# Kernel optimization log

Measured on AMD Instinct MI355X. Metric: run time of the kernel, lower is better.

## Reference

```python
import jax, jax.numpy as jnp
import numpy as np

B, N, C = 16, 3136, 576
HEADS, AG, WIN, PS = 8, 49, 56, 7


def setup_inputs() -> dict:
    key = jax.random.key(0)
    ks = jax.random.split(key, 14)
    std = 0.02
    d = {
        "x": jax.random.normal(ks[0], (B, N, C), jnp.float32),
        "Wq": std * jax.random.normal(ks[1], (C, C), jnp.float32),
        "Wkv": std * jax.random.normal(ks[2], (C, 2 * C), jnp.float32),
        "an_bias": std * jax.random.normal(ks[3], (HEADS, AG, 7, 7), jnp.float32),
        "na_bias": std * jax.random.normal(ks[4], (HEADS, AG, 7, 7), jnp.float32),
        "ah_bias": std * jax.random.normal(ks[5], (1, HEADS, AG, WIN, 1), jnp.float32),
        "aw_bias": std * jax.random.normal(ks[6], (1, HEADS, AG, 1, WIN), jnp.float32),
        "ha_bias": std * jax.random.normal(ks[7], (1, HEADS, WIN, 1, AG), jnp.float32),
        "wa_bias": std * jax.random.normal(ks[8], (1, HEADS, 1, WIN, AG), jnp.float32),
        "dwc_w": std * jax.random.normal(ks[9], (C, 1, 3, 3), jnp.float32),  # depthwise 3x3
        "dwc_gamma": jnp.ones((C,), jnp.float32),
        "dwc_beta": jnp.zeros((C,), jnp.float32),
        "proj_w": std * jax.random.normal(ks[10], (C, C), jnp.float32),
        "proj_b": jnp.zeros((C,), jnp.float32),
        "H": 56,
        "W": 56,
    }
    return d


def _forward(x, Wq, Wkv, an_bias, na_bias, ah_bias, aw_bias, ha_bias, wa_bias,
             dwc_w, dwc_gamma, dwc_beta, proj_w, proj_b, H, W):
    b, n, c = x.shape
    heads, ag = an_bias.shape[0], an_bias.shape[1]
    hd = c // heads
    scale = hd ** -0.5

    q = x @ Wq                     # [b, n, c]
    kv = x @ Wkv                   # [b, n, 2c]
    k, v = kv[..., :c], kv[..., c:]

    # agent tokens: adaptive avg pool q (H,W grid) down to (PS, PS)
    ps = int(round(ag ** 0.5))
    qa = q.reshape(b, ps, H // ps, ps, W // ps, c).mean(axis=(2, 4))  # [b, ps, ps, c]
    a = qa.reshape(b, ag, heads, hd).transpose(0, 2, 1, 3)            # [b, h, ag, hd]

    qh = q.reshape(b, n, heads, hd).transpose(0, 2, 1, 3)  # [b, h, n, hd]
    kh = k.reshape(b, n, heads, hd).transpose(0, 2, 1, 3)
    vh = v.reshape(b, n, heads, hd).transpose(0, 2, 1, 3)

    # stage 1: agent attends to K/V, with interpolated + separable position bias
    pb1 = jax.image.resize(an_bias, (heads, ag, H, W), "linear").reshape(1, heads, ag, n)
    pb2 = (ah_bias + aw_bias).reshape(1, heads, ag, n)
    agent_scores = jnp.einsum("bhad,bhnd->bhan", a * scale, kh) + pb1 + pb2
    agent_attn = jax.nn.softmax(agent_scores, axis=-1)
    agent_v = jnp.einsum("bhan,bhnd->bhad", agent_attn, vh)  # [b, h, ag, hd]

    # stage 2: queries attend to agent tokens
    ab1 = jax.image.resize(na_bias, (heads, ag, H, W), "linear").reshape(1, heads, ag, n)
    ab1 = ab1.transpose(0, 1, 3, 2)                                   # [1, h, n, ag]
    ab2 = (ha_bias + wa_bias).reshape(1, heads, n, ag)
    q_scores = jnp.einsum("bhnd,bhad->bhna", qh * scale, a) + ab1 + ab2
    q_attn = jax.nn.softmax(q_scores, axis=-1)
    out = jnp.einsum("bhna,bhad->bhnd", q_attn, agent_v)
    out = out.transpose(0, 2, 1, 3).reshape(b, n, c)

    # depthwise-conv branch on v (DW_bn_relu, BN in eval mode with unit stats)
    vimg = v.transpose(0, 2, 1).reshape(b, c, H, W)
    y = jax.lax.conv_general_dilated(vimg, dwc_w, (1, 1), "SAME",
                                     feature_group_count=c,
                                     dimension_numbers=("NCHW", "OIHW", "NCHW"))
    y = jax.nn.relu(y * dwc_gamma[None, :, None, None] + dwc_beta[None, :, None, None])
    y = y.reshape(b, c, n).transpose(0, 2, 1)

    out = out + y
    out = out @ proj_w + proj_b   # output projection
    return out


def reference(x, Wq, Wkv, an_bias, na_bias, ah_bias, aw_bias, ha_bias, wa_bias,
              dwc_w, dwc_gamma, dwc_beta, proj_w, proj_b, H, W):
    return _forward(x, Wq, Wkv, an_bias, na_bias, ah_bias, aw_bias, ha_bias, wa_bias,
                    dwc_w, dwc_gamma, dwc_beta, proj_w, proj_b, H, W)
```

## Files before the change

kernel.cpp:

```cpp
#include <hip/hip_runtime.h>
#include <stdint.h>

typedef unsigned short u16;
typedef u16   u16x4 __attribute__((ext_vector_type(4)));
typedef u16   u16x8 __attribute__((ext_vector_type(8)));
typedef float f32x4 __attribute__((ext_vector_type(4)));
typedef __bf16 bf16x8 __attribute__((ext_vector_type(8)));

#define BB    16
#define NN    3136
#define CC    576
#define HEADS 8
#define HD    72
#define AGN   49
#define NTOT  1728
#define NCH   7
#define SCALE 0.1178511301977579f

__device__ __forceinline__ u16 f2bf(float f) {
    unsigned u = __float_as_uint(f);
    return (u16)((u + 0x7fffu + ((u >> 16) & 1u)) >> 16);
}
__device__ __forceinline__ float bf2f(u16 u) {
    return __uint_as_float(((unsigned)u) << 16);
}

__global__ __launch_bounds__(256) void k_cast_x(const float* __restrict__ x, u16* __restrict__ xb) {
    size_t i = (size_t)blockIdx.x * 256 + threadIdx.x;
    f32x4 v = *(const f32x4*)(x + i * 4);
    u16x4 o; o[0] = f2bf(v[0]); o[1] = f2bf(v[1]); o[2] = f2bf(v[2]); o[3] = f2bf(v[3]);
    *(u16x4*)(xb + i * 4) = o;
}

__global__ __launch_bounds__(256) void k_prep_w(const float* __restrict__ Wq, const float* __restrict__ Wkv,
                                                const float* __restrict__ Wp,
                                                u16* __restrict__ wbT, u16* __restrict__ wpT) {
    int idx = blockIdx.x * 256 + threadIdx.x;
    if (idx < NTOT * CC) {
        int nn = idx / CC, kk = idx % CC;
        float v = (nn < CC) ? Wq[kk * CC + nn] : Wkv[kk * (2 * CC) + (nn - CC)];
        wbT[idx] = f2bf(v);
    } else {
        int j = idx - NTOT * CC;
        int nn = j / CC, kk = j % CC;
        wpT[j] = f2bf(Wp[kk * CC + nn]);
    }
}

__device__ __forceinline__ float bilerp7(const float* __restrict__ g, int oy, int ox) {
    float cy = (oy - 3.5f) * 0.125f;
    float cx = (ox - 3.5f) * 0.125f;
    float fy0 = floorf(cy), fx0 = floorf(cx);
    float ty = cy - fy0, tx = cx - fx0;
    int iy0 = (int)fy0, ix0 = (int)fx0;
    int y0 = min(6, max(0, iy0)), y1 = min(6, max(0, iy0 + 1));
    int x0 = min(6, max(0, ix0)), x1 = min(6, max(0, ix0 + 1));
    float g00 = g[y0 * 7 + x0], g01 = g[y0 * 7 + x1];
    float g10 = g[y1 * 7 + x0], g11 = g[y1 * 7 + x1];
    return (1.f - ty) * ((1.f - tx) * g00 + tx * g01) + ty * ((1.f - tx) * g10 + tx * g11);
}

__global__ __launch_bounds__(256) void k_bias1(const float* __restrict__ an, const float* __restrict__ ah,
                                               const float* __restrict__ aw, float* __restrict__ b1) {
    int idx = blockIdx.x * 256 + threadIdx.x;
    int ag = idx % AGN; int r = idx / AGN; int n = r % NN; int h = r / NN;
    int y = n / 56, x = n % 56;
    float v = bilerp7(an + (h * AGN + ag) * 49, y, x);
    b1[idx] = v + ah[(h * AGN + ag) * 56 + y] + aw[(h * AGN + ag) * 56 + x];
}

__global__ __launch_bounds__(256) void k_bias2(const float* __restrict__ na, const float* __restrict__ ha,
                                               const float* __restrict__ wa, float* __restrict__ b2p) {
    int idx = blockIdx.x * 256 + threadIdx.x;
    int ag = idx & 63; int r = idx >> 6; int n = r % NN; int h = r / NN;
    float v;
    if (ag < AGN) {
        int y = n / 56, x = n % 56;
        v = bilerp7(na + (h * AGN + ag) * 49, y, x)
          + ha[(h * 56 + y) * AGN + ag] + wa[(h * 56 + x) * AGN + ag];
    } else v = -1e30f;
    b2p[idx] = v;
}

template<int MODE>
__global__ __launch_bounds__(256) void k_gemm(const u16* __restrict__ A, const u16* __restrict__ Bt,
                                              u16* __restrict__ Qp, u16* __restrict__ Kp, u16* __restrict__ Vp,
                                              float* __restrict__ Cf, const float* __restrict__ bias,
                                              const int M) {
    const int NB = (MODE == 0) ? NTOT : CC;
    __shared__ u16 SMEM[2 * 128 * 64];
    u16* Asm = SMEM;
    u16* Bsm = SMEM + 128 * 64;
    const int t = threadIdx.x, lane = t & 63, wid = t >> 6;
    const int wm = wid & 1, wn = wid >> 1;
    const int nwg = gridDim.x * gridDim.y;
    const int id = blockIdx.y * gridDim.x + blockIdx.x;
    const int qq = nwg >> 3, rr = nwg & 7;
    const int xcd = id & 7, off = id >> 3;
    const int nid = (xcd < rr ? xcd * (qq + 1) : rr * (qq + 1) + (xcd - rr) * qq) + off;
    const int row0 = (nid / gridDim.x) * 128, col0 = (nid % gridDim.x) * 128;
    const int lr = lane & 15, lk = lane >> 4;
    f32x4 acc[4][4];
#pragma unroll
    for (int m = 0; m < 4; m++)
#pragma unroll
        for (int n2 = 0; n2 < 4; n2++) acc[m][n2] = (f32x4)0.f;

    for (int kt = 0; kt < 9; ++kt) {
        const int k0 = kt * 64;
#pragma unroll
        for (int it = 0; it < 4; ++it) {
            int flat = it * 256 + wid * 64 + lane;
            int r = flat >> 3, lc = (flat & 7) ^ (r & 7);
            int arow = (MODE == 0) ? (row0 + r) : min(row0 + r, M - 1);
            const u16* src = A + (size_t)arow * CC + k0 + lc * 8;
            __builtin_amdgcn_global_load_lds((const __attribute__((address_space(1))) void*)src,
                                             (__attribute__((address_space(3))) void*)(&Asm[(it * 256 + wid * 64) * 8]),
                                             16, 0, 0);
        }
#pragma unroll
        for (int it = 0; it < 4; ++it) {
            int flat = it * 256 + wid * 64 + lane;
            int r = flat >> 3, lc = (flat & 7) ^ (r & 7);
            int brow = min(col0 + r, NB - 1);
            const u16* src = Bt + (size_t)brow * CC + k0 + lc * 8;
            __builtin_amdgcn_global_load_lds((const __attribute__((address_space(1))) void*)src,
                                             (__attribute__((address_space(3))) void*)(&Bsm[(it * 256 + wid * 64) * 8]),
                                             16, 0, 0);
        }
        __syncthreads();
#pragma unroll
        for (int kk = 0; kk < 2; ++kk) {
            const int klocal2 = (kk * 32 + lk * 8) * 2;
            bf16x8 av[4], bv[4];
#pragma unroll
            for (int m = 0; m < 4; m++) {
                int row = wm * 64 + m * 16 + lr;
                av[m] = *(const bf16x8*)((const char*)Asm + row * 128 + (klocal2 ^ ((row & 7) << 4)));
            }
#pragma unroll
            for (int n2 = 0; n2 < 4; n2++) {
                int row = wn * 64 + n2 * 16 + lr;
                bv[n2] = *(const bf16x8*)((const char*)Bsm + row * 128 + (klocal2 ^ ((row & 7) << 4)));
            }
#pragma unroll
            for (int m = 0; m < 4; m++)
#pragma unroll
                for (int n2 = 0; n2 < 4; n2++)
                    acc[m][n2] = __builtin_amdgcn_mfma_f32_16x16x32_bf16(av[m], bv[n2], acc[m][n2], 0, 0, 0);
        }
        __syncthreads();
    }

    if (MODE == 0) {
#pragma unroll
        for (int ph = 0; ph < 2; ++ph) {
            if (wm == ph) {
#pragma unroll
                for (int m = 0; m < 4; m++)
#pragma unroll
                    for (int n2 = 0; n2 < 4; n2++) {
                        int col = wn * 64 + n2 * 16 + lr;
#pragma unroll
                        for (int j = 0; j < 4; j++)
                            SMEM[(m * 16 + lk * 4 + j) * 136 + col] = f2bf(acc[m][n2][j]);
                    }
            }
            __syncthreads();
#pragma unroll
            for (int cc2 = 0; cc2 < 4; ++cc2) {
                int cidx = cc2 * 256 + t;
                int rl = cidx >> 4, colc = cidx & 15;
                int cgl = col0 + colc * 8;
                if (cgl < NTOT) {
                    u16x8 v = *(const u16x8*)&SMEM[rl * 136 + colc * 8];
                    int rgl = row0 + ph * 64 + rl;
                    int which = cgl / 576, rem = cgl - which * 576;
                    int hh = rem / 72, dd = rem - hh * 72;
                    u16* dst = which == 0 ? Qp : (which == 1 ? Kp : Vp);
                    int b = rgl / NN, n = rgl - b * NN;
                    *(u16x8*)(dst + ((size_t)(b * 8 + hh) * NN + n) * 72 + dd) = v;
                }
            }
            __syncthreads();
        }
    } else {
        float* Ef = (float*)SMEM;
#pragma unroll
        for (int ph = 0; ph < 4; ++ph) {
            if (wm == (ph >> 1)) {
#pragma unroll
                for (int mm = 0; mm < 2; mm++) {
                    int m = (ph & 1) * 2 + mm;
#pragma unroll
                    for (int n2 = 0; n2 < 4; n2++) {
                        int col = wn * 64 + n2 * 16 + lr;
                        float addv = (MODE == 1) ? bias[min(col0 + col, NB - 1)] : 0.f;
#pragma unroll
                        for (int j = 0; j < 4; j++)
                            Ef[(mm * 16 + lk * 4 + j) * 136 + col] = acc[m][n2][j] + addv;
                    }
                }
            }
            __syncthreads();
#pragma unroll
            for (int cc2 = 0; cc2 < 4; ++cc2) {
                int cidx = cc2 * 256 + t;
                int rl = cidx >> 5, colc = cidx & 31;
                int cgl = col0 + colc * 4;
                int rgl = row0 + ph * 32 + rl;
                if (cgl < NB && rgl < M) {
                    f32x4 v = *(const f32x4*)&Ef[rl * 136 + colc * 4];
                    *(f32x4*)(Cf + (size_t)rgl * 576 + cgl) = v;
                }
            }
            __syncthreads();
        }
    }
}

__global__ __launch_bounds__(256) void k_poolx(const u16* __restrict__ xb, u16* __restrict__ px) {
    const int t = threadIdx.x;
    const int b = blockIdx.x / 7, p1 = blockIdx.x % 7;
    for (int task = t; task < 504; task += 256) {
        int p2 = task / 72, c8 = task - p2 * 72;
        const u16* base = xb + ((size_t)b * NN + (p1 * 8) * 56 + p2 * 8) * CC + c8 * 8;
        float s[8] = {0.f, 0.f, 0.f, 0.f, 0.f, 0.f, 0.f, 0.f};
        for (int y = 0; y < 8; ++y)
#pragma unroll
            for (int x = 0; x < 8; ++x) {
                u16x8 v = *(const u16x8*)(base + (size_t)(y * 56 + x) * CC);
#pragma unroll
                for (int j = 0; j < 8; j++) s[j] += bf2f(v[j]);
            }
        u16x8 o;
#pragma unroll
        for (int j = 0; j < 8; j++) o[j] = f2bf(s[j] * 0.015625f);
        *(u16x8*)(px + (size_t)(b * AGN + p1 * 7 + p2) * CC + c8 * 8) = o;
    }
}

__global__ __launch_bounds__(256) void k_stageA(const u16* __restrict__ Kp, const u16* __restrict__ Vp,
                                                const float* __restrict__ a_f, const float* __restrict__ b1,
                                                float* __restrict__ part) {
    const int t = threadIdx.x, lane = t & 63, w = t >> 6;
    const int c = lane & 15, g = lane >> 4;
    const int bh = blockIdx.y, b = bh >> 3, h = bh & 7;
    const int chunk = blockIdx.x;

    __shared__ u16 A_lds[64][104];
    __shared__ u16 K_lds[64][104];
    __shared__ u16 Vt[80][72];
    __shared__ u16 P_lds[64][72];

    for (int i = t; i < 64 * 104; i += 256) {
        int r = i / 104, cc = i - r * 104;
        if (cc >= 72 || r >= 49) A_lds[r][cc] = 0;
        if (cc >= 72) K_lds[r][cc] = 0;
    }
    for (int i = t; i < 8 * 72; i += 256) Vt[72 + i / 72][i % 72] = 0;
    for (int i = t; i < 49 * 72; i += 256) {
        int r = i / 72, d = i - r * 72;
        A_lds[r][d] = f2bf(a_f[(size_t)(b * 49 + r) * CC + h * 72 + d] * SCALE);
    }
    __syncthreads();

    bf16x8 bfA[3];
#pragma unroll
    for (int ks = 0; ks < 3; ++ks) bfA[ks] = *(const bf16x8*)&A_lds[16 * w + c][8 * g + 32 * ks];

    float m_run = -1e30f, l_run = 0.f;
    f32x4 acc[5];
#pragma unroll
    for (int dt = 0; dt < 5; ++dt) acc[dt] = (f32x4)0.f;

    const u16* kb = Kp + ((size_t)(b * 8 + h) * NN + chunk * 448) * 72;
    const u16* vb = Vp + ((size_t)(b * 8 + h) * NN + chunk * 448) * 72;
    const int arow = min(16 * w + c, 48);

    for (int tile = 0; tile < 7; ++tile) {
        for (int i = t; i < 576; i += 256) {
            int nl = i / 9, ch = i - nl * 9;
            u16x8 kd = *(const u16x8*)(kb + (size_t)tile * 4608 + i * 8);
            *(u16x8*)&K_lds[nl][ch * 8] = kd;
        }
        for (int i = t; i < 576; i += 256) {
            int ch = i >> 6, nl = i & 63;
            u16x8 vd = *(const u16x8*)(vb + (size_t)tile * 4608 + (nl * 9 + ch) * 8);
#pragma unroll
            for (int j = 0; j < 8; j++) Vt[ch * 8 + j][nl] = vd[j];
        }
        __syncthreads();

        f32x4 sT[4];
        const int nbase = chunk * 448 + tile * 64 + 4 * g;
#pragma unroll
        for (int nm = 0; nm < 4; ++nm) {
            f32x4 sv;
#pragma unroll
            for (int j = 0; j < 4; j++)
                sv[j] = b1[(size_t)(h * NN + nbase + 16 * nm + j) * AGN + arow];
#pragma unroll
            for (int ks = 0; ks < 3; ++ks) {
                bf16x8 af = *(const bf16x8*)&K_lds[16 * nm + c][8 * g + 32 * ks];
                sv = __builtin_amdgcn_mfma_f32_16x16x32_bf16(af, bfA[ks], sv, 0, 0, 0);
            }
            sT[nm] = sv;
        }

        float mt = sT[0][0];
#pragma unroll
        for (int nm = 0; nm < 4; ++nm)
#pragma unroll
            for (int j = 0; j < 4; j++) mt = fmaxf(mt, sT[nm][j]);
        mt = fmaxf(mt, __shfl_xor(mt, 16, 64));
        mt = fmaxf(mt, __shfl_xor(mt, 32, 64));
        float mnew = fmaxf(m_run, mt);
        float ps = 0.f;
#pragma unroll
        for (int nm = 0; nm < 4; ++nm) {
            float p0 = __expf(sT[nm][0] - mnew);
            float p1 = __expf(sT[nm][1] - mnew);
            float p2 = __expf(sT[nm][2] - mnew);
            float p3 = __expf(sT[nm][3] - mnew);
            ps += (p0 + p1) + (p2 + p3);
            unsigned pk01 = ((unsigned)f2bf(p1) << 16) | f2bf(p0);
            unsigned pk23 = ((unsigned)f2bf(p3) << 16) | f2bf(p2);
            unsigned* dst = (unsigned*)&P_lds[16 * w + c][16 * nm + 4 * g];
            dst[0] = pk01; dst[1] = pk23;
        }
        ps += __shfl_xor(ps, 16, 64);
        ps += __shfl_xor(ps, 32, 64);
        float rsc = __expf(m_run - mnew);
        l_run = l_run * rsc + ps;
        m_run = mnew;

        float rj[4];
#pragma unroll
        for (int j = 0; j < 4; j++) rj[j] = __shfl(rsc, 4 * g + j, 64);
        bf16x8 pa[2];
#pragma unroll
        for (int ks = 0; ks < 2; ++ks) pa[ks] = *(const bf16x8*)&P_lds[16 * w + c][8 * g + 32 * ks];
#pragma unroll
        for (int dt = 0; dt < 5; ++dt) {
            f32x4 a0 = acc[dt];
#pragma unroll
            for (int j = 0; j < 4; j++) a0[j] *= rj[j];
#pragma unroll
            for (int ks = 0; ks < 2; ++ks) {
                bf16x8 vf = *(const bf16x8*)&Vt[16 * dt + c][8 * g + 32 * ks];
                a0 = __builtin_amdgcn_mfma_f32_16x16x32_bf16(pa[ks], vf, a0, 0, 0, 0);
            }
            acc[dt] = a0;
        }
        __syncthreads();
    }

    const size_t pbase = (size_t)(bh * NCH + chunk) * (49 * 74);
#pragma unroll
    for (int dt = 0; dt < 5; ++dt) {
        int d = 16 * dt + c;
        if (d < 72) {
#pragma unroll
            for (int j = 0; j < 4; j++) {
                int agent = 16 * w + 4 * g + j;
                if (agent < 49) part[pbase + agent * 74 + d] = acc[dt][j];
            }
        }
    }
    if (g == 0) {
        int agent = 16 * w + c;
        if (agent < 49) {
            part[pbase + agent * 74 + 72] = m_run;
            part[pbase + agent * 74 + 73] = l_run;
        }
    }
}

__global__ __launch_bounds__(256) void k_reduceA(const float* __restrict__ part, float* __restrict__ agv) {
    const int bh = blockIdx.x, t = threadIdx.x;
    const float* pb = part + (size_t)bh * NCH * (49 * 74);
    for (int idx = t; idx < 49 * 72; idx += 256) {
        int row = idx / 72, d = idx - row * 72;
        float m = -1e30f;
#pragma unroll
        for (int c = 0; c < NCH; c++) m = fmaxf(m, pb[c * (49 * 74) + row * 74 + 72]);
        float accv = 0.f, l = 0.f;
#pragma unroll
        for (int c = 0; c < NCH; c++) {
            const float* pc = pb + c * (49 * 74) + row * 74;
            float e = __expf(pc[72] - m);
            accv += pc[d] * e;
            l += pc[73] * e;
        }
        agv[(size_t)(bh * 49 + row) * 72 + d] = accv / l;
    }
}

__global__ __launch_bounds__(256) void k_stageB(const u16* __restrict__ Qp, const float* __restrict__ a_f,
                                                const float* __restrict__ agv, const float* __restrict__ b2p,
                                                u16* __restrict__ oat) {
    const int t = threadIdx.x, lane = t & 63, w = t >> 6;
    const int c = lane & 15, g = lane >> 4;
    const int bh = blockIdx.y, b = bh >> 3, h = bh & 7;
    const int n0 = blockIdx.x * 256;

    __shared__ u16 A_lds[64][104];
    __shared__ u16 avT[80][72];
    __shared__ u16 Pt[4][64][76];

    for (int i = t; i < 64 * 104; i += 256) {
        int r = i / 104, cc = i - r * 104;
        if (cc >= 72 || r >= 49) A_lds[r][cc] = 0;
    }
    for (int i = t; i < 80 * 72; i += 256) ((u16*)avT)[i] = 0;
    __syncthreads();
    for (int i = t; i < 49 * 72; i += 256) {
        int r = i / 72, d = i - r * 72;
        A_lds[r][d] = f2bf(a_f[(size_t)(b * 49 + r) * CC + h * 72 + d] * SCALE);
        avT[d][r]   = f2bf(agv[(size_t)(bh * 49 + r) * 72 + d]);
    }
    __syncthreads();

    bf16x8 afr[4][3];
#pragma unroll
    for (int mt = 0; mt < 4; ++mt)
#pragma unroll
        for (int ks = 0; ks < 3; ++ks) afr[mt][ks] = *(const bf16x8*)&A_lds[16 * mt + c][8 * g + 32 * ks];

    const int nw0 = n0 + w * 64;
#pragma unroll
    for (int cg = 0; cg < 4; ++cg) {
        const int n = nw0 + 16 * cg + c;
        const int ne = min(n, NN - 1);
        const u16* qp = Qp + ((size_t)(b * 8 + h) * NN + ne) * 72;
        bf16x8 qf[3];
#pragma unroll
        for (int ks = 0; ks < 3; ++ks) qf[ks] = *(const bf16x8*)(qp + 8 * g + 32 * ks);
        const float* bp = b2p + (size_t)(h * NN + ne) * 64;
        f32x4 sv[4];
#pragma unroll
        for (int mt = 0; mt < 4; ++mt) sv[mt] = *(const f32x4*)(bp + 16 * mt + 4 * g);
#pragma unroll
        for (int ks = 0; ks < 3; ++ks)
#pragma unroll
            for (int mt = 0; mt < 4; ++mt)
                sv[mt] = __builtin_amdgcn_mfma_f32_16x16x32_bf16(afr[mt][ks], qf[ks], sv[mt], 0, 0, 0);
        float mx = sv[0][0];
#pragma unroll
        for (int mt = 0; mt < 4; ++mt)
#pragma unroll
            for (int j = 0; j < 4; j++) mx = fmaxf(mx, sv[mt][j]);
        mx = fmaxf(mx, __shfl_xor(mx, 16, 64));
        mx = fmaxf(mx, __shfl_xor(mx, 32, 64));
        float ps = 0.f;
#pragma unroll
        for (int mt = 0; mt < 4; ++mt) {
#pragma unroll
            for (int j = 0; j < 4; j++) { sv[mt][j] = __expf(sv[mt][j] - mx); ps += sv[mt][j]; }
        }
        ps += __shfl_xor(ps, 16, 64);
        ps += __shfl_xor(ps, 32, 64);
        float inv = 1.f / ps;
#pragma unroll
        for (int mt = 0; mt < 4; ++mt) {
            unsigned pk01 = ((unsigned)f2bf(sv[mt][1] * inv) << 16) | f2bf(sv[mt][0] * inv);
            unsigned pk23 = ((unsigned)f2bf(sv[mt][3] * inv) << 16) | f2bf(sv[mt][2] * inv);
            unsigned* dst = (unsigned*)&Pt[w][16 * cg + c][16 * mt + 4 * g];
            dst[0] = pk01; dst[1] = pk23;
        }
    }
    bf16x8 vfr[5][2];
#pragma unroll
    for (int dt = 0; dt < 5; ++dt)
#pragma unroll
        for (int ks = 0; ks < 2; ++ks) vfr[dt][ks] = *(const bf16x8*)&avT[16 * dt + c][8 * g + 32 * ks];
#pragma unroll
    for (int rt = 0; rt < 4; ++rt) {
        bf16x8 pf[2];
#pragma unroll
        for (int ks = 0; ks < 2; ++ks) pf[ks] = *(const bf16x8*)&Pt[w][16 * rt + c][8 * g + 32 * ks];
#pragma unroll
        for (int dt = 0; dt < 5; ++dt) {
            f32x4 a0 = (f32x4)0.f;
            a0 = __builtin_amdgcn_mfma_f32_16x16x32_bf16(pf[0], vfr[dt][0], a0, 0, 0, 0);
            a0 = __builtin_amdgcn_mfma_f32_16x16x32_bf16(pf[1], vfr[dt][1], a0, 0, 0, 0);
            int dd = 16 * dt + c;
            if (dd < 72) {
#pragma unroll
                for (int j = 0; j < 4; j++) {
                    int nn2 = nw0 + 16 * rt + 4 * g + j;
                    if (nn2 < NN) oat[((size_t)b * NN + nn2) * CC + h * 72 + dd] = f2bf(a0[j]);
                }
            }
        }
    }
}

__global__ __launch_bounds__(576) void k_conv(const u16* __restrict__ Vp, const u16* __restrict__ oat,
                                              const float* __restrict__ w, const float* __restrict__ gamma,
                                              const float* __restrict__ beta, u16* __restrict__ pre) {
    const int t = threadIdx.x;
    const int g8 = t % 72;
    const int p  = t / 72;
    const int c0 = g8 * 8;
    const int hh = c0 / 72, dl = c0 - hh * 72;

    __shared__ float wlds[CC * 9];
    __shared__ float glds[CC], blds[CC];
    for (int i = t; i < CC * 9; i += 576) wlds[i] = w[i];
    glds[t < CC ? t : 0] = gamma[t < CC ? t : 0];
    blds[t < CC ? t : 0] = beta[t < CC ? t : 0];
    __syncthreads();

    float wv[8][9], gm[8], bt[8];
#pragma unroll
    for (int j = 0; j < 8; j++) {
#pragma unroll
        for (int tap = 0; tap < 9; tap++) wv[j][tap] = wlds[(c0 + j) * 9 + tap];
        gm[j] = glds[c0 + j]; bt[j] = blds[c0 + j];
    }

    for (int pt = blockIdx.x * 8 + p; pt < BB * NN; pt += gridDim.x * 8) {
        int b = pt / NN, n = pt - b * NN;
        int y = n / 56, x = n % 56;
        const u16* vbase = Vp + ((size_t)(b * 8 + hh) * NN) * 72 + dl;
        float a[8] = {0.f, 0.f, 0.f, 0.f, 0.f, 0.f, 0.f, 0.f};
#pragma unroll
        for (int dy = -1; dy <= 1; ++dy) {
            int yy = y + dy; if (yy < 0 || yy > 55) continue;
#pragma unroll
            for (int dx = -1; dx <= 1; ++dx) {
                int xx = x + dx; if (xx < 0 || xx > 55) continue;
                u16x8 vv = *(const u16x8*)(vbase + (size_t)(yy * 56 + xx) * 72);
                int tap = (dy + 1) * 3 + (dx + 1);
#pragma unroll
                for (int j = 0; j < 8; j++) a[j] += bf2f(vv[j]) * wv[j][tap];
            }
        }
        u16x8 ov = *(const u16x8*)(oat + (size_t)pt * CC + c0);
        u16x8 rr;
#pragma unroll
        for (int j = 0; j < 8; j++)
            rr[j] = f2bf(bf2f(ov[j]) + fmaxf(a[j] * gm[j] + bt[j], 0.f));
        *(u16x8*)(pre + (size_t)pt * CC + c0) = rr;
    }
}

extern "C" void kernel_launch(void* const* d_in, const int* in_sizes, int n_in,
                              void* d_out, int out_size, void* d_ws, size_t ws_size,
                              hipStream_t stream) {
    const float* x     = (const float*)d_in[0];
    const float* Wq    = (const float*)d_in[1];
    const float* Wkv   = (const float*)d_in[2];
    const float* an_b  = (const float*)d_in[3];
    const float* na_b  = (const float*)d_in[4];
    const float* ah_b  = (const float*)d_in[5];
    const float* aw_b  = (const float*)d_in[6];
    const float* ha_b  = (const float*)d_in[7];
    const float* wa_b  = (const float*)d_in[8];
    const float* dwcw  = (const float*)d_in[9];
    const float* gam   = (const float*)d_in[10];
    const float* bet   = (const float*)d_in[11];
    const float* projw = (const float*)d_in[12];
    const float* projb = (const float*)d_in[13];
    float* out = (float*)d_out;

    char* ws = (char*)d_ws;
    u16* wbT  = (u16*)(ws + 0);
    u16* wpT  = (u16*)(ws + 1990656);
    u16* xb   = (u16*)(ws + 2654208);
    u16* Qp   = (u16*)(ws + 60456960);
    u16* Kp   = (u16*)(ws + 118259712);
    u16* Vp   = (u16*)(ws + 176062464);
    float* af = (float*)(ws + 233865216);
    u16* px   = (u16*)(ws + 235671552);
    float* agv= (float*)(ws + 235671552);
    float* b1 = (float*)(ws + 237477888);
    float* b2p= (float*)(ws + 242395136);
    float* part = (float*)xb;
    u16* obuf = Kp;

    k_cast_x<<<28224, 256, 0, stream>>>(x, xb);
    k_prep_w<<<5184, 256, 0, stream>>>(Wq, Wkv, projw, wbT, wpT);
    k_bias1<<<4802, 256, 0, stream>>>(an_b, ah_b, aw_b, b1);
    k_bias2<<<6272, 256, 0, stream>>>(na_b, ha_b, wa_b, b2p);
    k_poolx<<<112, 256, 0, stream>>>(xb, px);
    k_gemm<2><<<dim3(5, 7), 256, 0, stream>>>(px, wbT, nullptr, nullptr, nullptr, af, nullptr, 784);
    k_gemm<0><<<dim3(14, 392), 256, 0, stream>>>(xb, wbT, Qp, Kp, Vp, nullptr, nullptr, BB * NN);
    k_stageA<<<dim3(NCH, 128), 256, 0, stream>>>(Kp, Vp, af, b1, part);
    k_reduceA<<<128, 256, 0, stream>>>(part, agv);
    k_stageB<<<dim3(13, 128), 256, 0, stream>>>(Qp, af, agv, b2p, obuf);
    k_conv<<<784, 576, 0, stream>>>(Vp, obuf, dwcw, gam, bet, xb );
    k_gemm<1><<<dim3(5, 392), 256, 0, stream>>>(xb , wpT, nullptr, nullptr, nullptr, out, projb, BB * NN);
}
```

Baseline: 552.0 us.

## Write QKV epilogue directly from registers and rebalance stage-A chunking

The QKV GEMM epilogue drops the LDS staging and its barriers. Each lane now writes its accumulator elements straight to the head-split Q/K/V buffers as scalar 2-byte stores, and the A-row index is clamped for every mode. Stage A splits the 49 K/V tiles into 6 chunks (9 tiles, then 8 each) instead of 7 chunks of 7 tiles, so fewer blocks each carry more work. The scalar stores give up coalescing in exchange for removing the shared-memory round trip, and the new chunk count must agree with the downstream combine kernel.

```diff
diff --git a/kernel.cpp b/kernel.cpp
--- a/kernel.cpp
+++ b/kernel.cpp
@@ -14,7 +14,7 @@
 #define HD    72
 #define AGN   49
 #define NTOT  1728
-#define NCH   7
+#define NCH   6
 #define SCALE 0.1178511301977579f
 
 __device__ __forceinline__ u16 f2bf(float f) {
@@ -112,7 +112,7 @@
         for (int it = 0; it < 4; ++it) {
             int flat = it * 256 + wid * 64 + lane;
             int r = flat >> 3, lc = (flat & 7) ^ (r & 7);
-            int arow = (MODE == 0) ? (row0 + r) : min(row0 + r, M - 1);
+            int arow = min(row0 + r, M - 1);
             const u16* src = A + (size_t)arow * CC + k0 + lc * 8;
             __builtin_amdgcn_global_load_lds((const __attribute__((address_space(1))) void*)src,
                                              (__attribute__((address_space(3))) void*)(&Asm[(it * 256 + wid * 64) * 8]),
@@ -154,35 +154,22 @@
 
     if (MODE == 0) {
 #pragma unroll
-        for (int ph = 0; ph < 2; ++ph) {
-            if (wm == ph) {
-#pragma unroll
-                for (int m = 0; m < 4; m++)
-#pragma unroll
-                    for (int n2 = 0; n2 < 4; n2++) {
-                        int col = wn * 64 + n2 * 16 + lr;
-#pragma unroll
-                        for (int j = 0; j < 4; j++)
-                            SMEM[(m * 16 + lk * 4 + j) * 136 + col] = f2bf(acc[m][n2][j]);
-                    }
-            }
-            __syncthreads();
-#pragma unroll
-            for (int cc2 = 0; cc2 < 4; ++cc2) {
-                int cidx = cc2 * 256 + t;
-                int rl = cidx >> 4, colc = cidx & 15;
-                int cgl = col0 + colc * 8;
-                if (cgl < NTOT) {
-                    u16x8 v = *(const u16x8*)&SMEM[rl * 136 + colc * 8];
-                    int rgl = row0 + ph * 64 + rl;
-                    int which = cgl / 576, rem = cgl - which * 576;
-                    int hh = rem / 72, dd = rem - hh * 72;
-                    u16* dst = which == 0 ? Qp : (which == 1 ? Kp : Vp);
+        for (int n2 = 0; n2 < 4; n2++) {
+            int cgl = col0 + wn * 64 + n2 * 16 + lr;
+            if (cgl >= NB) continue;
+            int which = cgl / 576;
+            int rem = cgl - which * 576;
+            int hh = rem / 72;
+            int dd = rem - hh * 72;
+            u16* dst = which == 0 ? Qp : (which == 1 ? Kp : Vp);
+#pragma unroll
+            for (int m = 0; m < 4; m++)
+#pragma unroll
+                for (int j = 0; j < 4; j++) {
+                    int rgl = row0 + wm * 64 + m * 16 + lk * 4 + j;
                     int b = rgl / NN, n = rgl - b * NN;
-                    *(u16x8*)(dst + ((size_t)(b * 8 + hh) * NN + n) * 72 + dd) = v;
+                    dst[((size_t)(b * 8 + hh) * NN + n) * 72 + dd] = f2bf(acc[m][n2][j]);
                 }
-            }
-            __syncthreads();
         }
     } else {
         float* Ef = (float*)SMEM;
@@ -247,6 +234,8 @@
     const int c = lane & 15, g = lane >> 4;
     const int bh = blockIdx.y, b = bh >> 3, h = bh & 7;
     const int chunk = blockIdx.x;
+    const int t0 = (chunk == 0) ? 0 : 9 + 8 * (chunk - 1);
+    const int ntile = (chunk == 0) ? 9 : 8;
 
     __shared__ u16 A_lds[64][104];
     __shared__ u16 K_lds[64][104];
@@ -274,11 +263,11 @@
 #pragma unroll
     for (int dt = 0; dt < 5; ++dt) acc[dt] = (f32x4)0.f;
 
-    const u16* kb = Kp + ((size_t)(b * 8 + h) * NN + chunk * 448) * 72;
-    const u16* vb = Vp + ((size_t)(b * 8 + h) * NN + chunk * 448) * 72;
+    const u16* kb = Kp + ((size_t)(b * 8 + h) * NN + t0 * 64) * 72;
+    const u16* vb = Vp + ((size_t)(b * 8 + h) * NN + t0 * 64) * 72;
     const int arow = min(16 * w + c, 48);
 
-    for (int tile = 0; tile < 7; ++tile) {
+    for (int tile = 0; tile < ntile; ++tile) {
         for (int i = t; i < 576; i += 256) {
             int nl = i / 9, ch = i - nl * 9;
             u16x8 kd = *(const u16x8*)(kb + (size_t)tile * 4608 + i * 8);
@@ -293,7 +282,7 @@
         __syncthreads();
 
         f32x4 sT[4];
-        const int nbase = chunk * 448 + tile * 64 + 4 * g;
+        const int nbase = (t0 + tile) * 64 + 4 * g;
 #pragma unroll
         for (int nm = 0; nm < 4; ++nm) {
             f32x4 sv;
```

Result: faster. 520.4 us (-5.7%).
